# Optimization experiments

Hardware: AMD Instinct MI355X
Metric: run time of the kernel (lower is better)

## Reference

```python
import jax, jax.numpy as jnp
import numpy as np

B, N, T, D = 8, 64, 50, 4      # batch, atoms, timesteps, features per node
K, H = 2, 64                   # edge types, hidden (msg_hid = msg_out = n_hid)
START = 1                      # skip_first_edge_type=True
E = N * (N - 1)


def setup_inputs() -> dict:
    key = jax.random.key(0)
    ks = jax.random.split(key, 10)
    # fully-connected relation graph: all ordered pairs i != j
    recv_idx, send_idx = np.where(~np.eye(N, dtype=bool))
    eye = np.eye(N, dtype=np.float32)
    rel_rec = jnp.asarray(eye[recv_idx])    # [E, N] one-hot receivers
    rel_send = jnp.asarray(eye[send_idx])   # [E, N] one-hot senders
    s = 0.1
    return {
        "inputs": jax.random.normal(ks[0], (B, N, T, D), jnp.float32),
        "rel_type": jax.random.uniform(ks[1], (B, 1, E, K), jnp.float32),
        "rel_rec": rel_rec,
        "rel_send": rel_send,
        "fc1_w": jax.random.normal(ks[2], (K, H, 2 * D), jnp.float32) * s,
        "fc1_b": jnp.zeros((K, H), jnp.float32),
        "fc2_w": jax.random.normal(ks[3], (K, H, H), jnp.float32) * s,
        "fc2_b": jnp.zeros((K, H), jnp.float32),
        "out1_w": jax.random.normal(ks[4], (H, D + H), jnp.float32) * s,
        "out1_b": jnp.zeros((H,), jnp.float32),
        "out2_w": jax.random.normal(ks[5], (H, H), jnp.float32) * s,
        "out2_b": jnp.zeros((H,), jnp.float32),
        "out3_w": jax.random.normal(ks[6], (D, H), jnp.float32) * s,
        "out3_b": jnp.zeros((D,), jnp.float32),
        "pred_steps": 1,
    }


def reference(inputs, rel_type, rel_rec, rel_send,
              fc1_w, fc1_b, fc2_w, fc2_b,
              out1_w, out1_b, out2_w, out2_b, out3_w, out3_b,
              pred_steps):
    assert pred_steps == 1
    x_in = jnp.swapaxes(inputs, 1, 2)  # [B, T, N, D]
    t = x_in.shape[1]
    # rel_type [B,1,E,K] -> expand over time
    rt = jnp.broadcast_to(rel_type, (rel_type.shape[0], t) + rel_type.shape[2:])

    # node2edge: gather receivers/senders via one-hot matmuls
    recv = jnp.einsum('en,btnd->bted', rel_rec, x_in)
    send = jnp.einsum('en,btnd->bted', rel_send, x_in)
    pre_msg = jnp.concatenate([recv, send], axis=-1)  # [B,T,E,2D]

    # per-edge-type MLP, masked by inferred edge prob, accumulated
    all_msgs = jnp.zeros(pre_msg.shape[:3] + (H,), pre_msg.dtype)
    for i in range(START, K):
        h = jax.nn.relu(jnp.einsum('bted,hd->bteh', pre_msg, fc1_w[i]) + fc1_b[i])
        m = jax.nn.relu(jnp.einsum('bteh,oh->bteo', h, fc2_w[i]) + fc2_b[i])
        all_msgs = all_msgs + m * rt[..., i:i + 1]

    # edge2node: scatter-accumulate to receivers via one-hot transpose matmul
    agg = jnp.einsum('en,bteh->btnh', rel_rec, all_msgs)  # [B,T,N,H]

    aug = jnp.concatenate([x_in, agg], axis=-1)           # [B,T,N,D+H]
    h = jax.nn.relu(jnp.einsum('btni,oi->btno', aug, out1_w) + out1_b)
    h = jax.nn.relu(jnp.einsum('btni,oi->btno', h, out2_w) + out2_b)
    delta = jnp.einsum('btni,oi->btno', h, out3_w) + out3_b
    x_tp1 = x_in + delta                                  # predict_delta=True

    pred_all = x_tp1[:, :t - 1]                           # [B,T-1,N,D]
    return jnp.swapaxes(pred_all, 1, 2)                   # [B,N,T-1,D]
```

## Files before the change

### kernel.cpp

```cpp
#include <hip/hip_runtime.h>


#define NB 8
#define NN 64
#define NT 50
#define NTO 49
#define ND 4
#define NE 4032

typedef _Float16 f16x8 __attribute__((ext_vector_type(8)));
typedef _Float16 f16x4 __attribute__((ext_vector_type(4)));
typedef _Float16 f16x2 __attribute__((ext_vector_type(2)));
typedef float f32x4 __attribute__((ext_vector_type(4)));
typedef float f32x2 __attribute__((ext_vector_type(2)));

union Frag8 { unsigned u[4]; f16x8 f; f16x2 h[4]; };

__device__ __forceinline__ unsigned pk16(float lo, float hi) {
  return __builtin_bit_cast(unsigned, __builtin_amdgcn_cvt_pkrtz(lo, hi));
}

__device__ __forceinline__ void lds_fence() {
  __builtin_amdgcn_sched_barrier(0);
  asm volatile("s_waitcnt lgkmcnt(0)" ::: "memory");
  __builtin_amdgcn_sched_barrier(0);
}

#define MFMA16(A, B, C) __builtin_amdgcn_mfma_f32_16x16x32_f16((A), (B), (C), 0, 0, 0)

__global__ __launch_bounds__(256) void nri_fused_kernel(
    const float* __restrict__ inputs,
    const float* __restrict__ rel_type,
    const float* __restrict__ fc1_w,
    const float* __restrict__ fc1_b,
    const float* __restrict__ fc2_w,
    const float* __restrict__ fc2_b,
    const float* __restrict__ out1_w,
    const float* __restrict__ out1_b,
    const float* __restrict__ out2_w,
    const float* __restrict__ out2_b,
    const float* __restrict__ out3_w,
    const float* __restrict__ out3_b,
    float* __restrict__ out)
{
  __shared__ __align__(16) char smem[15872];
  _Float16* const Vh   = (_Float16*)(smem);
  _Float16* const Ph   = (_Float16*)(smem + 9216);
  _Float16* const Rl   = (_Float16*)(smem + 11264);
  float4*   const Xl   = (float4*)  (smem + 13312);
  _Float16* const AggL = (_Float16*)(smem + 13568);

  const int bid    = blockIdx.x;
  const int tile   = bid & 3;
  const int t      = (bid >> 2) % NTO;
  const int b      = bid / (4 * NTO);
  const int n_base = tile * 16;
  const int tid  = threadIdx.x;
  const int lane = tid & 63;
  const int w    = tid >> 6;
  const int q    = lane >> 4;
  const int r    = lane & 15;

  {
    const int k = lane;
    const float4 w1r = *(const float4*)(fc1_w + 512 + k * 8);
    const float4 w1s = *(const float4*)(fc1_w + 516 + k * 8);
    const float  b1k = fc1_b[64 + k];
#pragma unroll
    for (int ii = 0; ii < 16; ++ii) {
      const int i = ii * 4 + w;
      const float4 x = *(const float4*)(inputs + ((b * NN + i) * NT + t) * ND);
      Vh[i * 72 + k] = (_Float16)(w1s.x*x.x + w1s.y*x.y + w1s.z*x.z + w1s.w*x.w);
    }
#pragma unroll
    for (int ii = 0; ii < 4; ++ii) {
      const int i = ii * 4 + w;
      const float4 x = *(const float4*)(inputs + ((b * NN + n_base + i) * NT + t) * ND);
      Ph[i * 64 + k] = (_Float16)(b1k + w1r.x*x.x + w1r.y*x.y + w1r.z*x.z + w1r.w*x.w);
    }
  }
#pragma unroll
  for (int ii = 0; ii < 4; ++ii) {
    const int idx = ii * 256 + tid;
    const int i = idx >> 6, s = idx & 63;
    const int n = n_base + i;
    const float v = (s == n) ? 0.f
                  : rel_type[(b * NE + n * 63 + (s < n ? s : s - 1)) * 2 + 1];
    Rl[idx] = (_Float16)v;
  }
  if (tid < 16)
    Xl[tid] = *(const float4*)(inputs + ((b * NN + n_base + tid) * NT + t) * ND);

  Frag8 bfr[4][2];
  float b2l[4];
#pragma unroll
  for (int nt = 0; nt < 4; ++nt) {
    const int o = nt * 16 + r;
    b2l[nt] = fc2_b[64 + o];
#pragma unroll
    for (int ks = 0; ks < 2; ++ks) {
      const float* p = fc2_w + 4096 + o * 64 + ks * 32 + q * 8;
      const float4 c0 = *(const float4*)p;
      const float4 c1 = *(const float4*)(p + 4);
      bfr[nt][ks].u[0] = pk16(c0.x, c0.y);
      bfr[nt][ks].u[1] = pk16(c0.z, c0.w);
      bfr[nt][ks].u[2] = pk16(c1.x, c1.y);
      bfr[nt][ks].u[3] = pk16(c1.z, c1.w);
    }
  }
  __syncthreads();

#pragma unroll 1
  for (int np = 0; np < 4; ++np) {
    const int ni = w * 4 + np;
    Frag8 pa0, pa1;
    pa0.f = *(const f16x8*)(Ph + ni * 64 + q * 8);
    pa1.f = *(const f16x8*)(Ph + ni * 64 + 32 + q * 8);

    Frag8 va0, va1;
    {
      const _Float16* vp = Vh + r * 72 + q * 8;
      va0.f = *(const f16x8*)vp;
      va1.f = *(const f16x8*)(vp + 32);
    }

    float ag[4] = {0.f, 0.f, 0.f, 0.f};
#pragma unroll
    for (int st = 0; st < 4; ++st) {
      Frag8 nva0, nva1;
      if (st < 3) {
        const _Float16* vp = Vh + ((st + 1) * 16 + r) * 72 + q * 8;
        nva0.f = *(const f16x8*)vp;
        nva1.f = *(const f16x8*)(vp + 32);
      }

      const f16x4 rt4 = *(const f16x4*)(Rl + ni * 64 + st * 16 + q * 4);

      Frag8 a0, a1;
      const f16x2 z = {(_Float16)0.f, (_Float16)0.f};
#pragma unroll
      for (int j = 0; j < 4; ++j) {
        a0.h[j] = __builtin_elementwise_max((f16x2)(pa0.h[j] + va0.h[j]), z);
        a1.h[j] = __builtin_elementwise_max((f16x2)(pa1.h[j] + va1.h[j]), z);
      }

      __builtin_amdgcn_s_setprio(1);
      const f32x4 z4 = {0.f, 0.f, 0.f, 0.f};
#pragma unroll
      for (int nt = 0; nt < 4; ++nt) {
        f32x4 d = {b2l[nt], b2l[nt], b2l[nt], b2l[nt]};
        d = MFMA16(a0.f, bfr[nt][0].f, d);
        d = MFMA16(a1.f, bfr[nt][1].f, d);
        const f32x4 p = __builtin_elementwise_max(d, z4);
        float s = ag[nt];
        s += (float)rt4[0] * p[0];
        s += (float)rt4[1] * p[1];
        s += (float)rt4[2] * p[2];
        s += (float)rt4[3] * p[3];
        ag[nt] = s;
      }
      __builtin_amdgcn_s_setprio(0);

      va0 = nva0; va1 = nva1;
    }

#pragma unroll
    for (int nt = 0; nt < 4; ++nt) {
      float s = ag[nt];
      s += __shfl_xor(s, 16); s += __shfl_xor(s, 32);
      ag[nt] = s;
    }
    const float aval = (q == 0) ? ag[0] : (q == 1) ? ag[1] : (q == 2) ? ag[2] : ag[3];
    AggL[ni * 72 + lane] = (_Float16)aval;
  }

  __syncthreads();

  _Float16* const Reg = AggL + (w * 4) * 72;
  const float* const xf = (const float*)Xl;

  {
    Frag8 B1f[4][2]; float b1v[4]; float4 w1xv[4];
#pragma unroll
    for (int nt = 0; nt < 4; ++nt) {
      const int o = nt * 16 + r;
      b1v[nt]  = out1_b[o];
      w1xv[nt] = *(const float4*)(out1_w + o * 68);
#pragma unroll
      for (int ks = 0; ks < 2; ++ks) {
        const float* p1 = out1_w + o * 68 + 4 + ks * 32 + q * 8;
        const float4 c0 = *(const float4*)p1;
        const float4 c1 = *(const float4*)(p1 + 4);
        B1f[nt][ks].u[0] = pk16(c0.x, c0.y); B1f[nt][ks].u[1] = pk16(c0.z, c0.w);
        B1f[nt][ks].u[2] = pk16(c1.x, c1.y); B1f[nt][ks].u[3] = pk16(c1.z, c1.w);
      }
    }
    Frag8 A0, A1;
    A0.f = *(const f16x8*)(Reg + (r & 3) * 72 + q * 8);
    A1.f = *(const f16x8*)(Reg + (r & 3) * 72 + 32 + q * 8);
    f32x4 d0 = {b1v[0], b1v[0], b1v[0], b1v[0]};
    f32x4 d1 = {b1v[1], b1v[1], b1v[1], b1v[1]};
    f32x4 d2 = {b1v[2], b1v[2], b1v[2], b1v[2]};
    f32x4 d3 = {b1v[3], b1v[3], b1v[3], b1v[3]};
    d0 = MFMA16(A0.f, B1f[0][0].f, d0); d0 = MFMA16(A1.f, B1f[0][1].f, d0);
    d1 = MFMA16(A0.f, B1f[1][0].f, d1); d1 = MFMA16(A1.f, B1f[1][1].f, d1);
    d2 = MFMA16(A0.f, B1f[2][0].f, d2); d2 = MFMA16(A1.f, B1f[2][1].f, d2);
    d3 = MFMA16(A0.f, B1f[3][0].f, d3); d3 = MFMA16(A1.f, B1f[3][1].f, d3);
    if (q == 0) {
#pragma unroll
      for (int reg = 0; reg < 4; ++reg) {
        const int n = w * 4 + reg;
        const float4 x = Xl[n];
        const float xv0 = x.x*w1xv[0].x + x.y*w1xv[0].y + x.z*w1xv[0].z + x.w*w1xv[0].w;
        const float xv1 = x.x*w1xv[1].x + x.y*w1xv[1].y + x.z*w1xv[1].z + x.w*w1xv[1].w;
        const float xv2 = x.x*w1xv[2].x + x.y*w1xv[2].y + x.z*w1xv[2].z + x.w*w1xv[2].w;
        const float xv3 = x.x*w1xv[3].x + x.y*w1xv[3].y + x.z*w1xv[3].z + x.w*w1xv[3].w;
        Reg[reg * 72 +  0 + r] = (_Float16)fmaxf(d0[reg] + xv0, 0.f);
        Reg[reg * 72 + 16 + r] = (_Float16)fmaxf(d1[reg] + xv1, 0.f);
        Reg[reg * 72 + 32 + r] = (_Float16)fmaxf(d2[reg] + xv2, 0.f);
        Reg[reg * 72 + 48 + r] = (_Float16)fmaxf(d3[reg] + xv3, 0.f);
      }
    }
  }
  lds_fence();

  {
    Frag8 B2f[4][2]; float b2v[4];
#pragma unroll
    for (int nt = 0; nt < 4; ++nt) {
      const int o = nt * 16 + r;
      b2v[nt] = out2_b[o];
#pragma unroll
      for (int ks = 0; ks < 2; ++ks) {
        const float* p2 = out2_w + o * 64 + ks * 32 + q * 8;
        const float4 e0 = *(const float4*)p2;
        const float4 e1 = *(const float4*)(p2 + 4);
        B2f[nt][ks].u[0] = pk16(e0.x, e0.y); B2f[nt][ks].u[1] = pk16(e0.z, e0.w);
        B2f[nt][ks].u[2] = pk16(e1.x, e1.y); B2f[nt][ks].u[3] = pk16(e1.z, e1.w);
      }
    }
    Frag8 A0, A1;
    A0.f = *(const f16x8*)(Reg + (r & 3) * 72 + q * 8);
    A1.f = *(const f16x8*)(Reg + (r & 3) * 72 + 32 + q * 8);
    f32x4 d0 = {b2v[0], b2v[0], b2v[0], b2v[0]};
    f32x4 d1 = {b2v[1], b2v[1], b2v[1], b2v[1]};
    f32x4 d2 = {b2v[2], b2v[2], b2v[2], b2v[2]};
    f32x4 d3 = {b2v[3], b2v[3], b2v[3], b2v[3]};
    d0 = MFMA16(A0.f, B2f[0][0].f, d0); d0 = MFMA16(A1.f, B2f[0][1].f, d0);
    d1 = MFMA16(A0.f, B2f[1][0].f, d1); d1 = MFMA16(A1.f, B2f[1][1].f, d1);
    d2 = MFMA16(A0.f, B2f[2][0].f, d2); d2 = MFMA16(A1.f, B2f[2][1].f, d2);
    d3 = MFMA16(A0.f, B2f[3][0].f, d3); d3 = MFMA16(A1.f, B2f[3][1].f, d3);
    if (q == 0) {
#pragma unroll
      for (int reg = 0; reg < 4; ++reg) {
        Reg[reg * 72 +  0 + r] = (_Float16)fmaxf(d0[reg], 0.f);
        Reg[reg * 72 + 16 + r] = (_Float16)fmaxf(d1[reg], 0.f);
        Reg[reg * 72 + 32 + r] = (_Float16)fmaxf(d2[reg], 0.f);
        Reg[reg * 72 + 48 + r] = (_Float16)fmaxf(d3[reg], 0.f);
      }
    }
  }
  lds_fence();

  {
    Frag8 B3f[2];
#pragma unroll
    for (int ks = 0; ks < 2; ++ks) {
      const float* p3 = out3_w + (r & 3) * 64 + ks * 32 + q * 8;
      const float4 c0 = *(const float4*)p3;
      const float4 c1 = *(const float4*)(p3 + 4);
      B3f[ks].u[0] = pk16(c0.x, c0.y); B3f[ks].u[1] = pk16(c0.z, c0.w);
      B3f[ks].u[2] = pk16(c1.x, c1.y); B3f[ks].u[3] = pk16(c1.z, c1.w);
    }
    Frag8 A0, A1;
    A0.f = *(const f16x8*)(Reg + (r & 3) * 72 + q * 8);
    A1.f = *(const f16x8*)(Reg + (r & 3) * 72 + 32 + q * 8);
    const float b3o = out3_b[r & 3];
    f32x4 d = {b3o, b3o, b3o, b3o};
    d = MFMA16(A0.f, B3f[0].f, d);
    d = MFMA16(A1.f, B3f[1].f, d);
    if (q == 0 && r < 4) {
#pragma unroll
      for (int reg = 0; reg < 4; ++reg) {
        const int n = w * 4 + reg;
        out[((b * NN + n_base + n) * NTO + t) * ND + r] = xf[n * 4 + r] + d[reg];
      }
    }
  }
}

extern "C" void kernel_launch(void* const* d_in, const int* in_sizes, int n_in,
                              void* d_out, int out_size, void* d_ws, size_t ws_size,
                              hipStream_t stream) {
  const float* inputs   = (const float*)d_in[0];
  const float* rel_type = (const float*)d_in[1];
  const float* fc1_w  = (const float*)d_in[4];
  const float* fc1_b  = (const float*)d_in[5];
  const float* fc2_w  = (const float*)d_in[6];
  const float* fc2_b  = (const float*)d_in[7];
  const float* out1_w = (const float*)d_in[8];
  const float* out1_b = (const float*)d_in[9];
  const float* out2_w = (const float*)d_in[10];
  const float* out2_b = (const float*)d_in[11];
  const float* out3_w = (const float*)d_in[12];
  const float* out3_b = (const float*)d_in[13];
  float* out = (float*)d_out;

  nri_fused_kernel<<<NB * NTO * 4, 256, 0, stream>>>(
      inputs, rel_type, fc1_w, fc1_b, fc2_w, fc2_b,
      out1_w, out1_b, out2_w, out2_b, out3_w, out3_b, out);
}
```

Measured before the change: 128.1 us.

## Make each wave self-contained with private LDS slices and drop block barriers

Each wave now owns a private LDS region holding its own receiver projections, edge weights, aggregates and node features, so the two __syncthreads are replaced by wave-local lgkmcnt fences. The sender-side fc1 projection is computed straight into register fragments per lane instead of being staged in a shared LDS table. All output-MLP weights are loaded into registers before the message loop. This removes block-wide synchronisation and shrinks LDS use, but raises register pressure and repeats the sender projection work in every wave.

```diff
diff --git a/kernel.cpp b/kernel.cpp
--- a/kernel.cpp
+++ b/kernel.cpp
@@ -12,7 +12,6 @@
 typedef _Float16 f16x4 __attribute__((ext_vector_type(4)));
 typedef _Float16 f16x2 __attribute__((ext_vector_type(2)));
 typedef float f32x4 __attribute__((ext_vector_type(4)));
-typedef float f32x2 __attribute__((ext_vector_type(2)));
 
 union Frag8 { unsigned u[4]; f16x8 f; f16x2 h[4]; };
 
@@ -43,12 +42,7 @@
     const float* __restrict__ out3_b,
     float* __restrict__ out)
 {
-  __shared__ __align__(16) char smem[15872];
-  _Float16* const Vh   = (_Float16*)(smem);
-  _Float16* const Ph   = (_Float16*)(smem + 9216);
-  _Float16* const Rl   = (_Float16*)(smem + 11264);
-  float4*   const Xl   = (float4*)  (smem + 13312);
-  _Float16* const AggL = (_Float16*)(smem + 13568);
+  __shared__ __align__(16) char smem[6656];
 
   const int bid    = blockIdx.x;
   const int tile   = bid & 3;
@@ -61,35 +55,55 @@
   const int q    = lane >> 4;
   const int r    = lane & 15;
 
+  char* const ws = smem + w * 1664;
+  _Float16* const RlW = (_Float16*)ws;
+  _Float16* const PhW = (_Float16*)(ws + 512);
+  _Float16* const Reg = (_Float16*)(ws + 1024);
+  float4*   const XW  = (float4*)(ws + 1600);
+
   {
     const int k = lane;
     const float4 w1r = *(const float4*)(fc1_w + 512 + k * 8);
-    const float4 w1s = *(const float4*)(fc1_w + 516 + k * 8);
     const float  b1k = fc1_b[64 + k];
 #pragma unroll
-    for (int ii = 0; ii < 16; ++ii) {
-      const int i = ii * 4 + w;
-      const float4 x = *(const float4*)(inputs + ((b * NN + i) * NT + t) * ND);
-      Vh[i * 72 + k] = (_Float16)(w1s.x*x.x + w1s.y*x.y + w1s.z*x.z + w1s.w*x.w);
-    }
-#pragma unroll
     for (int ii = 0; ii < 4; ++ii) {
-      const int i = ii * 4 + w;
-      const float4 x = *(const float4*)(inputs + ((b * NN + n_base + i) * NT + t) * ND);
-      Ph[i * 64 + k] = (_Float16)(b1k + w1r.x*x.x + w1r.y*x.y + w1r.z*x.z + w1r.w*x.w);
-    }
-  }
-#pragma unroll
-  for (int ii = 0; ii < 4; ++ii) {
-    const int idx = ii * 256 + tid;
-    const int i = idx >> 6, s = idx & 63;
-    const int n = n_base + i;
+      const int n = n_base + w * 4 + ii;
+      const float4 x = *(const float4*)(inputs + ((b * NN + n) * NT + t) * ND);
+      PhW[ii * 64 + k] = (_Float16)(b1k + w1r.x*x.x + w1r.y*x.y + w1r.z*x.z + w1r.w*x.w);
+    }
+  }
+#pragma unroll
+  for (int j = 0; j < 4; ++j) {
+    const int e = lane * 4 + j;
+    const int ii = e >> 6, s = e & 63;
+    const int n = n_base + w * 4 + ii;
     const float v = (s == n) ? 0.f
                   : rel_type[(b * NE + n * 63 + (s < n ? s : s - 1)) * 2 + 1];
-    Rl[idx] = (_Float16)v;
-  }
-  if (tid < 16)
-    Xl[tid] = *(const float4*)(inputs + ((b * NN + n_base + tid) * NT + t) * ND);
+    RlW[e] = (_Float16)v;
+  }
+  if (lane < 4)
+    XW[lane] = *(const float4*)(inputs + ((b * NN + n_base + w * 4 + lane) * NT + t) * ND);
+
+  Frag8 vr[4][2];
+  {
+    float4 w1sv[16];
+#pragma unroll
+    for (int f = 0; f < 2; ++f)
+#pragma unroll
+      for (int j = 0; j < 8; ++j)
+        w1sv[f * 8 + j] = *(const float4*)(fc1_w + 516 + (f * 32 + q * 8 + j) * 8);
+#pragma unroll
+    for (int st = 0; st < 4; ++st) {
+      const float4 xs = *(const float4*)(inputs + ((b * NN + st * 16 + r) * NT + t) * ND);
+#pragma unroll
+      for (int f = 0; f < 2; ++f)
+#pragma unroll
+        for (int j = 0; j < 8; ++j) {
+          const float4 ww = w1sv[f * 8 + j];
+          vr[st][f].f[j] = (_Float16)(ww.x*xs.x + ww.y*xs.y + ww.z*xs.z + ww.w*xs.w);
+        }
+    }
+  }
 
   Frag8 bfr[4][2];
   float b2l[4];
@@ -108,40 +122,59 @@
       bfr[nt][ks].u[3] = pk16(c1.z, c1.w);
     }
   }
-  __syncthreads();
+
+  Frag8 B1f[4][2], B2f[4][2], B3f[2];
+  float b1v[4], b2v[4];
+  float4 w1xv[4];
+#pragma unroll
+  for (int nt = 0; nt < 4; ++nt) {
+    const int o = nt * 16 + r;
+    b1v[nt]  = out1_b[o];
+    b2v[nt]  = out2_b[o];
+    w1xv[nt] = *(const float4*)(out1_w + o * 68);
+#pragma unroll
+    for (int ks = 0; ks < 2; ++ks) {
+      const float* p1 = out1_w + o * 68 + 4 + ks * 32 + q * 8;
+      const float4 c0 = *(const float4*)p1;
+      const float4 c1 = *(const float4*)(p1 + 4);
+      B1f[nt][ks].u[0] = pk16(c0.x, c0.y); B1f[nt][ks].u[1] = pk16(c0.z, c0.w);
+      B1f[nt][ks].u[2] = pk16(c1.x, c1.y); B1f[nt][ks].u[3] = pk16(c1.z, c1.w);
+      const float* p2 = out2_w + o * 64 + ks * 32 + q * 8;
+      const float4 e0 = *(const float4*)p2;
+      const float4 e1 = *(const float4*)(p2 + 4);
+      B2f[nt][ks].u[0] = pk16(e0.x, e0.y); B2f[nt][ks].u[1] = pk16(e0.z, e0.w);
+      B2f[nt][ks].u[2] = pk16(e1.x, e1.y); B2f[nt][ks].u[3] = pk16(e1.z, e1.w);
+    }
+  }
+#pragma unroll
+  for (int ks = 0; ks < 2; ++ks) {
+    const float* p3 = out3_w + (r & 3) * 64 + ks * 32 + q * 8;
+    const float4 c0 = *(const float4*)p3;
+    const float4 c1 = *(const float4*)(p3 + 4);
+    B3f[ks].u[0] = pk16(c0.x, c0.y); B3f[ks].u[1] = pk16(c0.z, c0.w);
+    B3f[ks].u[2] = pk16(c1.x, c1.y); B3f[ks].u[3] = pk16(c1.z, c1.w);
+  }
+  const float b3o = out3_b[r & 3];
+
+  lds_fence();
 
 #pragma unroll 1
   for (int np = 0; np < 4; ++np) {
-    const int ni = w * 4 + np;
     Frag8 pa0, pa1;
-    pa0.f = *(const f16x8*)(Ph + ni * 64 + q * 8);
-    pa1.f = *(const f16x8*)(Ph + ni * 64 + 32 + q * 8);
-
-    Frag8 va0, va1;
-    {
-      const _Float16* vp = Vh + r * 72 + q * 8;
-      va0.f = *(const f16x8*)vp;
-      va1.f = *(const f16x8*)(vp + 32);
-    }
+    pa0.f = *(const f16x8*)(PhW + np * 64 + q * 8);
+    pa1.f = *(const f16x8*)(PhW + np * 64 + 32 + q * 8);
 
     float ag[4] = {0.f, 0.f, 0.f, 0.f};
 #pragma unroll
     for (int st = 0; st < 4; ++st) {
-      Frag8 nva0, nva1;
-      if (st < 3) {
-        const _Float16* vp = Vh + ((st + 1) * 16 + r) * 72 + q * 8;
-        nva0.f = *(const f16x8*)vp;
-        nva1.f = *(const f16x8*)(vp + 32);
-      }
-
-      const f16x4 rt4 = *(const f16x4*)(Rl + ni * 64 + st * 16 + q * 4);
+      const f16x4 rt4 = *(const f16x4*)(RlW + np * 64 + st * 16 + q * 4);
 
       Frag8 a0, a1;
       const f16x2 z = {(_Float16)0.f, (_Float16)0.f};
 #pragma unroll
       for (int j = 0; j < 4; ++j) {
-        a0.h[j] = __builtin_elementwise_max((f16x2)(pa0.h[j] + va0.h[j]), z);
-        a1.h[j] = __builtin_elementwise_max((f16x2)(pa1.h[j] + va1.h[j]), z);
+        a0.h[j] = __builtin_elementwise_max((f16x2)(pa0.h[j] + vr[st][0].h[j]), z);
+        a1.h[j] = __builtin_elementwise_max((f16x2)(pa1.h[j] + vr[st][1].h[j]), z);
       }
 
       __builtin_amdgcn_s_setprio(1);
@@ -160,8 +193,6 @@
         ag[nt] = s;
       }
       __builtin_amdgcn_s_setprio(0);
-
-      va0 = nva0; va1 = nva1;
     }
 
 #pragma unroll
@@ -171,30 +202,12 @@
       ag[nt] = s;
     }
     const float aval = (q == 0) ? ag[0] : (q == 1) ? ag[1] : (q == 2) ? ag[2] : ag[3];
-    AggL[ni * 72 + lane] = (_Float16)aval;
-  }
-
-  __syncthreads();
-
-  _Float16* const Reg = AggL + (w * 4) * 72;
-  const float* const xf = (const float*)Xl;
-
-  {
-    Frag8 B1f[4][2]; float b1v[4]; float4 w1xv[4];
-#pragma unroll
-    for (int nt = 0; nt < 4; ++nt) {
-      const int o = nt * 16 + r;
-      b1v[nt]  = out1_b[o];
-      w1xv[nt] = *(const float4*)(out1_w + o * 68);
-#pragma unroll
-      for (int ks = 0; ks < 2; ++ks) {
-        const float* p1 = out1_w + o * 68 + 4 + ks * 32 + q * 8;
-        const float4 c0 = *(const float4*)p1;
-        const float4 c1 = *(const float4*)(p1 + 4);
-        B1f[nt][ks].u[0] = pk16(c0.x, c0.y); B1f[nt][ks].u[1] = pk16(c0.z, c0.w);
-        B1f[nt][ks].u[2] = pk16(c1.x, c1.y); B1f[nt][ks].u[3] = pk16(c1.z, c1.w);
-      }
-    }
+    Reg[np * 72 + lane] = (_Float16)aval;
+  }
+
+  lds_fence();
+
+  {
     Frag8 A0, A1;
     A0.f = *(const f16x8*)(Reg + (r & 3) * 72 + q * 8);
     A1.f = *(const f16x8*)(Reg + (r & 3) * 72 + 32 + q * 8);
@@ -209,8 +222,7 @@
     if (q == 0) {
 #pragma unroll
       for (int reg = 0; reg < 4; ++reg) {
-        const int n = w * 4 + reg;
-        const float4 x = Xl[n];
+        const float4 x = XW[reg];
         const float xv0 = x.x*w1xv[0].x + x.y*w1xv[0].y + x.z*w1xv[0].z + x.w*w1xv[0].w;
         const float xv1 = x.x*w1xv[1].x + x.y*w1xv[1].y + x.z*w1xv[1].z + x.w*w1xv[1].w;
         const float xv2 = x.x*w1xv[2].x + x.y*w1xv[2].y + x.z*w1xv[2].z + x.w*w1xv[2].w;
@@ -225,20 +237,6 @@
   lds_fence();
 
   {
-    Frag8 B2f[4][2]; float b2v[4];
-#pragma unroll
-    for (int nt = 0; nt < 4; ++nt) {
-      const int o = nt * 16 + r;
-      b2v[nt] = out2_b[o];
-#pragma unroll
-      for (int ks = 0; ks < 2; ++ks) {
-        const float* p2 = out2_w + o * 64 + ks * 32 + q * 8;
-        const float4 e0 = *(const float4*)p2;
-        const float4 e1 = *(const float4*)(p2 + 4);
-        B2f[nt][ks].u[0] = pk16(e0.x, e0.y); B2f[nt][ks].u[1] = pk16(e0.z, e0.w);
-        B2f[nt][ks].u[2] = pk16(e1.x, e1.y); B2f[nt][ks].u[3] = pk16(e1.z, e1.w);
-      }
-    }
     Frag8 A0, A1;
     A0.f = *(const f16x8*)(Reg + (r & 3) * 72 + q * 8);
     A1.f = *(const f16x8*)(Reg + (r & 3) * 72 + 32 + q * 8);
@@ -263,27 +261,18 @@
   lds_fence();
 
   {
-    Frag8 B3f[2];
-#pragma unroll
-    for (int ks = 0; ks < 2; ++ks) {
-      const float* p3 = out3_w + (r & 3) * 64 + ks * 32 + q * 8;
-      const float4 c0 = *(const float4*)p3;
-      const float4 c1 = *(const float4*)(p3 + 4);
-      B3f[ks].u[0] = pk16(c0.x, c0.y); B3f[ks].u[1] = pk16(c0.z, c0.w);
-      B3f[ks].u[2] = pk16(c1.x, c1.y); B3f[ks].u[3] = pk16(c1.z, c1.w);
-    }
     Frag8 A0, A1;
     A0.f = *(const f16x8*)(Reg + (r & 3) * 72 + q * 8);
     A1.f = *(const f16x8*)(Reg + (r & 3) * 72 + 32 + q * 8);
-    const float b3o = out3_b[r & 3];
     f32x4 d = {b3o, b3o, b3o, b3o};
     d = MFMA16(A0.f, B3f[0].f, d);
     d = MFMA16(A1.f, B3f[1].f, d);
     if (q == 0 && r < 4) {
+      const float* xw = (const float*)XW;
 #pragma unroll
       for (int reg = 0; reg < 4; ++reg) {
         const int n = w * 4 + reg;
-        out[((b * NN + n_base + n) * NTO + t) * ND + r] = xf[n * 4 + r] + d[reg];
+        out[((b * NN + n_base + n) * NTO + t) * ND + r] = xw[reg * 4 + r] + d[reg];
       }
     }
   }
```

Measured after the change: 155.0 us. 21.0% more time.
